# Kernel optimization log

Measured on AMD Instinct MI355X. Metric: run time of the kernel, lower is better.

## Reference

```python
import jax, jax.numpy as jnp
import numpy as np

MODEL_DIM = 1024
HIDDEN = 2048
NUM_GROUPS = 2
EXPERTS_PER_GP = 4
NUM_EXPERTS = NUM_GROUPS * EXPERTS_PER_GP
TOP_K = 2
B, T = 2, 2048


def _swiglu(x):
    a, b = jnp.split(x, 2, axis=-1)
    return jax.nn.silu(a) * b


def setup_inputs() -> dict:
    key = jax.random.key(0)
    ks = jax.random.split(key, 7)
    s = 0.02  # init scale
    return {
        "x": jax.random.normal(ks[0], (B, T, MODEL_DIM), jnp.float32),
        # torch Linear weight layout [out_features, in_features]
        "w_in": jax.random.normal(ks[1], (HIDDEN * 2, MODEL_DIM), jnp.float32) * s,   # shared_in
        "w_out": jax.random.normal(ks[2], (MODEL_DIM, HIDDEN), jnp.float32) * s,      # shared_out
        "w1": jax.random.normal(ks[3], (HIDDEN * 2, MODEL_DIM), jnp.float32) * s,     # w1_shared
        "w2": jax.random.normal(ks[4], (NUM_EXPERTS, MODEL_DIM, HIDDEN), jnp.float32) * s,  # w2_expert stack
        "wg": jax.random.normal(ks[5], (NUM_GROUPS, MODEL_DIM), jnp.float32) * s,     # group_gate
        "we": jax.random.normal(ks[6], (NUM_EXPERTS, MODEL_DIM), jnp.float32) * s,    # expert_gate
        "gb": jnp.zeros((NUM_GROUPS,), jnp.float32),   # group_bias
        "eb": jnp.zeros((NUM_EXPERTS,), jnp.float32),  # expert_bias
    }


def reference(x, w_in, w_out, w1, w2, wg, we, gb, eb):
    Bs, Ts, C = x.shape
    S = Bs * Ts
    flat = x.reshape(S, C)

    # shared expert path
    shared = _swiglu(flat @ w_in.T) @ w_out.T                    # [S, C]

    # level-1: group gate (top-1)
    g_probs = jax.nn.softmax(flat @ wg.T + gb, axis=-1)          # [S, G]
    g_idx = jnp.argmax(g_probs, axis=-1)                         # [S]

    # level-2: expert gate masked to the chosen group
    e_logits = flat @ we.T + eb                                  # [S, E]
    egid = jnp.arange(NUM_EXPERTS) // EXPERTS_PER_GP             # expert -> group id
    masked = jnp.where(g_idx[:, None] == egid[None, :], e_logits, -jnp.inf)
    e_probs = jax.nn.softmax(masked, axis=-1)                    # zero outside group

    g_prob = jnp.take_along_axis(g_probs, g_idx[:, None], axis=1)  # [S, 1]
    p_expert = e_probs * g_prob                                  # [S, E]

    topv, topi = jax.lax.top_k(p_expert, TOP_K)                  # [S, k]

    # per-token per-expert combine weight (dense [S, E], rows k-sparse)
    w_se = jnp.zeros((S, NUM_EXPERTS), x.dtype).at[
        jnp.arange(S)[:, None], topi].add(topv)

    # w1 is shared across experts -> compute hidden once for all tokens
    h = _swiglu(flat @ w1.T)                                     # [S, H]

    # routed = sum_e w_se[:, e] * (h @ w2[e].T); scale commutes through linear
    routed = jnp.zeros_like(shared)
    for e in range(NUM_EXPERTS):  # small fixed expert count
        routed = routed + (h * w_se[:, e:e + 1]) @ w2[e].T

    return (shared + routed).reshape(Bs, Ts, C)
```

## Files before the change

### kernel.cpp

```cpp
#include <hip/hip_runtime.h>
#include <math.h>


#define C_DIM 1024
#define H_DIM 2048
#define S_TOK 4096

typedef _Float16 f16x8 __attribute__((ext_vector_type(8)));
typedef float f32x4 __attribute__((ext_vector_type(4)));

#define AS3(p) ((__attribute__((address_space(3))) void*)(p))
#define AS1c(p) ((const __attribute__((address_space(1))) void*)(p))

__global__ __launch_bounds__(256) void cvt_all(
    const float* __restrict__ x, const float* __restrict__ w_in,
    const float* __restrict__ w1, const float* __restrict__ w_out,
    const float* __restrict__ w2, _Float16* __restrict__ xh,
    _Float16* __restrict__ winh, _Float16* __restrict__ w1h,
    _Float16* __restrict__ wouth, _Float16* __restrict__ w2h) {
  int i = blockIdx.x * 256 + threadIdx.x;
  const float* s; _Float16* d; int off;
  if (i < 524288)        { s = x;     d = xh;    off = i; }
  else if (i < 1048576)  { s = w_in;  d = winh;  off = i - 524288; }
  else if (i < 1572864)  { s = w1;    d = w1h;   off = i - 1048576; }
  else if (i < 1835008)  { s = w_out; d = wouth; off = i - 1572864; }
  else                   { s = w2;    d = w2h;   off = i - 1835008; }
  const float4* sp = reinterpret_cast<const float4*>(s) + (size_t)off * 2;
  float4 a = sp[0], b = sp[1];
  f16x8 h;
  h[0] = (_Float16)a.x; h[1] = (_Float16)a.y; h[2] = (_Float16)a.z; h[3] = (_Float16)a.w;
  h[4] = (_Float16)b.x; h[5] = (_Float16)b.y; h[6] = (_Float16)b.z; h[7] = (_Float16)b.w;
  reinterpret_cast<f16x8*>(d)[off] = h;
}

__global__ __launch_bounds__(256) void gate_kernel(const float* __restrict__ x,
    const float* __restrict__ wg, const float* __restrict__ we,
    const float* __restrict__ gb, const float* __restrict__ eb,
    int* __restrict__ top2_e, float* __restrict__ top2_w) {
  const int lane = threadIdx.x & 63;
  const int token = blockIdx.x * 4 + (threadIdx.x >> 6);
  const float* xr = x + (size_t)token * C_DIM + lane * 16;
  float xv[16];
#pragma unroll
  for (int i = 0; i < 16; i += 4) {
    float4 t = *reinterpret_cast<const float4*>(xr + i);
    xv[i] = t.x; xv[i + 1] = t.y; xv[i + 2] = t.z; xv[i + 3] = t.w;
  }
  float dots[10];
#pragma unroll
  for (int g = 0; g < 10; ++g) {
    const float* wr = (g < 2 ? wg + (size_t)g * C_DIM : we + (size_t)(g - 2) * C_DIM) + lane * 16;
    float d = 0.f;
#pragma unroll
    for (int i = 0; i < 16; i += 4) {
      float4 t = *reinterpret_cast<const float4*>(wr + i);
      d += xv[i] * t.x + xv[i + 1] * t.y + xv[i + 2] * t.z + xv[i + 3] * t.w;
    }
#pragma unroll
    for (int off = 32; off > 0; off >>= 1) d += __shfl_xor(d, off);
    dots[g] = d;
  }
  if (lane != 0) return;
  float g0 = dots[0] + gb[0], g1 = dots[1] + gb[1];
  int gidx = (g0 >= g1) ? 0 : 1;
  float gm = fmaxf(g0, g1);
  float ex0 = expf(g0 - gm), ex1 = expf(g1 - gm);
  float gprob = (gidx == 0 ? ex0 : ex1) / (ex0 + ex1);
  const int base = gidx * 4;
  float el[4];
  float m = -1e30f;
#pragma unroll
  for (int j = 0; j < 4; ++j) { el[j] = dots[2 + base + j] + eb[base + j]; m = fmaxf(m, el[j]); }
  float s = 0.f;
#pragma unroll
  for (int j = 0; j < 4; ++j) { el[j] = expf(el[j] - m); s += el[j]; }
  float p[8];
#pragma unroll
  for (int e = 0; e < 8; ++e) p[e] = 0.f;
#pragma unroll
  for (int j = 0; j < 4; ++j) p[base + j] = el[j] / s * gprob;
  int i1 = 0; float v1 = -1.f;
#pragma unroll
  for (int e = 0; e < 8; ++e) if (p[e] > v1) { v1 = p[e]; i1 = e; }
  int i2 = -1; float v2 = -1.f;
#pragma unroll
  for (int e = 0; e < 8; ++e) if (e != i1 && p[e] > v2) { v2 = p[e]; i2 = e; }
  top2_e[token * 2] = i1;     top2_w[token * 2] = v1;
  top2_e[token * 2 + 1] = i2; top2_w[token * 2 + 1] = v2;
}

__global__ __launch_bounds__(256) void scanfill(const int* __restrict__ top2_e,
    const float* __restrict__ top2_w, int* __restrict__ offs_g,
    int* __restrict__ tok_list, float* __restrict__ scale_list,
    int* __restrict__ tok2slot) {
  __shared__ int cnt[8], offs[9], cur[8];
  const int tid = threadIdx.x;
  if (tid < 8) { cnt[tid] = 0; cur[tid] = 0; }
  __syncthreads();
  for (int i = tid; i < 2 * S_TOK; i += 256) atomicAdd(&cnt[top2_e[i]], 1);
  __syncthreads();
  if (tid == 0) {
    offs[0] = 0;
    for (int e = 0; e < 8; ++e) offs[e + 1] = offs[e] + cnt[e];
    for (int e = 0; e < 9; ++e) offs_g[e] = offs[e];
  }
  __syncthreads();
  for (int i = tid; i < 2 * S_TOK; i += 256) {
    int e = top2_e[i];
    int slot = atomicAdd(&cur[e], 1);
    int g = offs[e] + slot;
    tok_list[g] = i >> 1;
    scale_list[g] = top2_w[i];
    tok2slot[i] = g;
  }
}

__device__ __forceinline__ void stage_tile(_Float16* lds, const _Float16* src,
                                           int ld, int tid) {
#pragma unroll
  for (int i = 0; i < 2; ++i) {
    int c = tid + i * 512;
    int row = c >> 3;
    int u = c & 7;
    const _Float16* g = src + (size_t)row * ld + ((u ^ (row & 7)) << 3);
    _Float16* l = lds + ((c & ~63) << 3);
    __builtin_amdgcn_global_load_lds(AS1c(g), AS3(l), 16, 0, 0);
  }
}

__device__ __forceinline__ f16x8 frag_ld(const _Float16* t, int row, int u) {
  return *reinterpret_cast<const f16x8*>(t + row * 64 + ((u ^ (row & 7)) << 3));
}

__global__ __launch_bounds__(512) void gemm_swiglu(const _Float16* __restrict__ A,
    const _Float16* __restrict__ W, _Float16* __restrict__ H) {
  __shared__ _Float16 At[128 * 64];
  __shared__ _Float16 Ba[128 * 64];
  __shared__ _Float16 Bb[128 * 64];
  const int tid = threadIdx.x;
  const int lane = tid & 63;
  const int wid = tid >> 6;
  const int wm = wid >> 2;
  const int wn = wid & 3;
  const int row0 = blockIdx.x * 128;
  const int col0 = blockIdx.y * 128;

  f32x4 accA[4][2] = {};
  f32x4 accB[4][2] = {};

  for (int kt = 0; kt < C_DIM; kt += 64) {
    stage_tile(At, A + (size_t)row0 * C_DIM + kt, C_DIM, tid);
    stage_tile(Ba, W + (size_t)col0 * C_DIM + kt, C_DIM, tid);
    stage_tile(Bb, W + (size_t)(col0 + H_DIM) * C_DIM + kt, C_DIM, tid);
    __syncthreads();
#pragma unroll
    for (int ks = 0; ks < 2; ++ks) {
      const int u = (ks << 2) + (lane >> 4);
      f16x8 af[4], ba[2], bb[2];
#pragma unroll
      for (int m = 0; m < 4; ++m)
        af[m] = frag_ld(At, wm * 64 + m * 16 + (lane & 15), u);
#pragma unroll
      for (int n = 0; n < 2; ++n) {
        ba[n] = frag_ld(Ba, wn * 32 + n * 16 + (lane & 15), u);
        bb[n] = frag_ld(Bb, wn * 32 + n * 16 + (lane & 15), u);
      }
#pragma unroll
      for (int m = 0; m < 4; ++m)
#pragma unroll
        for (int n = 0; n < 2; ++n) {
          accA[m][n] = __builtin_amdgcn_mfma_f32_16x16x32_f16(af[m], ba[n], accA[m][n], 0, 0, 0);
          accB[m][n] = __builtin_amdgcn_mfma_f32_16x16x32_f16(af[m], bb[n], accB[m][n], 0, 0, 0);
        }
    }
    __syncthreads();
  }
#pragma unroll
  for (int m = 0; m < 4; ++m)
#pragma unroll
    for (int n = 0; n < 2; ++n)
#pragma unroll
      for (int r = 0; r < 4; ++r) {
        int row = row0 + wm * 64 + m * 16 + ((lane >> 4) << 2) + r;
        int col = col0 + wn * 32 + n * 16 + (lane & 15);
        float a = accA[m][n][r];
        float b = accB[m][n][r];
        float hval = (a / (1.0f + expf(-a))) * b;
        H[(size_t)row * H_DIM + col] = (_Float16)hval;
      }
}

__global__ __launch_bounds__(512) void gemm_out(
    const _Float16* __restrict__ H1, const _Float16* __restrict__ H2,
    const _Float16* __restrict__ Wout, const _Float16* __restrict__ W2,
    const int* __restrict__ offs_g, const int* __restrict__ tok_list,
    const float* __restrict__ scale_list,
    float* __restrict__ out, _Float16* __restrict__ routed) {
  __shared__ _Float16 At[128 * 64];
  __shared__ _Float16 Bt[128 * 64];
  __shared__ float sse[128];
  const int tid = threadIdx.x;
  const int lane = tid & 63;
  const int wid = tid >> 6;
  const int wm = wid >> 2, wn = wid & 3;

  const int b = blockIdx.x;
  const bool shared_role = (b < 256);
  int rb, cb, offs_e = 0, n_e = 0;
  const _Float16* Bp;
  if (shared_role) {
    rb = b >> 3; cb = b & 7;
    Bp = Wout;
  } else {
    int eb = b - 256;
    int e = eb >> 8; rb = (eb >> 3) & 31; cb = eb & 7;
    offs_e = offs_g[e]; n_e = offs_g[e + 1] - offs_e;
    if (rb * 128 >= n_e) return;
    Bp = W2 + (size_t)e * C_DIM * H_DIM;
    if (tid < 128) {
      int lr = rb * 128 + tid;
      sse[tid] = (lr < n_e) ? scale_list[offs_e + lr] : 0.f;
    }
  }

  const _Float16* aptr[2];
  _Float16* ldst[2];
#pragma unroll
  for (int i = 0; i < 2; ++i) {
    int c = tid + i * 512;
    int row = c >> 3, u = c & 7;
    int swz = (u ^ (row & 7)) << 3;
    const _Float16* rowbase;
    if (shared_role) {
      rowbase = H1 + (size_t)(rb * 128 + row) * H_DIM;
    } else {
      int lr = rb * 128 + row;
      int gs = offs_e + (lr < n_e ? lr : n_e - 1);
      rowbase = H2 + (size_t)tok_list[gs] * H_DIM;
    }
    aptr[i] = rowbase + swz;
    ldst[i] = At + ((c & ~63) << 3);
  }

  f32x4 acc[4][2] = {};
  for (int kt = 0; kt < H_DIM; kt += 64) {
#pragma unroll
    for (int i = 0; i < 2; ++i)
      __builtin_amdgcn_global_load_lds(AS1c(aptr[i] + kt), AS3(ldst[i]), 16, 0, 0);
    stage_tile(Bt, Bp + (size_t)cb * 128 * H_DIM + kt, H_DIM, tid);
    __syncthreads();
#pragma unroll
    for (int ks = 0; ks < 2; ++ks) {
      const int u = (ks << 2) + (lane >> 4);
      f16x8 af[4], bf[2];
#pragma unroll
      for (int m = 0; m < 4; ++m)
        af[m] = frag_ld(At, wm * 64 + m * 16 + (lane & 15), u);
#pragma unroll
      for (int n = 0; n < 2; ++n)
        bf[n] = frag_ld(Bt, wn * 32 + n * 16 + (lane & 15), u);
#pragma unroll
      for (int m = 0; m < 4; ++m)
#pragma unroll
        for (int n = 0; n < 2; ++n)
          acc[m][n] = __builtin_amdgcn_mfma_f32_16x16x32_f16(af[m], bf[n], acc[m][n], 0, 0, 0);
    }
    __syncthreads();
  }

#pragma unroll
  for (int m = 0; m < 4; ++m)
#pragma unroll
    for (int n = 0; n < 2; ++n)
#pragma unroll
      for (int r = 0; r < 4; ++r) {
        int rloc = wm * 64 + m * 16 + ((lane >> 4) << 2) + r;
        int col = cb * 128 + wn * 32 + n * 16 + (lane & 15);
        if (shared_role) {
          out[(size_t)(rb * 128 + rloc) * C_DIM + col] = acc[m][n][r];
        } else {
          int lr = rb * 128 + rloc;
          if (lr < n_e)
            routed[(size_t)(offs_e + lr) * C_DIM + col] =
                (_Float16)(sse[rloc] * acc[m][n][r]);
        }
      }
}

__global__ __launch_bounds__(256) void combine_final(float* __restrict__ out,
    const _Float16* __restrict__ routed, const int* __restrict__ tok2slot) {
  const int t = blockIdx.x * 2 + (threadIdx.x >> 7);
  const int cp = (threadIdx.x & 127) << 3;
  const int s0 = tok2slot[t * 2], s1 = tok2slot[t * 2 + 1];
  f16x8 r0 = *reinterpret_cast<const f16x8*>(routed + (size_t)s0 * C_DIM + cp);
  f16x8 r1 = *reinterpret_cast<const f16x8*>(routed + (size_t)s1 * C_DIM + cp);
  float* op = out + (size_t)t * C_DIM + cp;
  float4 o0 = *reinterpret_cast<const float4*>(op);
  float4 o1 = *reinterpret_cast<const float4*>(op + 4);
  o0.x += (float)r0[0] + (float)r1[0];
  o0.y += (float)r0[1] + (float)r1[1];
  o0.z += (float)r0[2] + (float)r1[2];
  o0.w += (float)r0[3] + (float)r1[3];
  o1.x += (float)r0[4] + (float)r1[4];
  o1.y += (float)r0[5] + (float)r1[5];
  o1.z += (float)r0[6] + (float)r1[6];
  o1.w += (float)r0[7] + (float)r1[7];
  *reinterpret_cast<float4*>(op) = o0;
  *reinterpret_cast<float4*>(op + 4) = o1;
}

extern "C" void kernel_launch(void* const* d_in, const int* in_sizes, int n_in,
                              void* d_out, int out_size, void* d_ws, size_t ws_size,
                              hipStream_t stream) {
  const float* x     = (const float*)d_in[0];
  const float* w_in  = (const float*)d_in[1];
  const float* w_out = (const float*)d_in[2];
  const float* w1    = (const float*)d_in[3];
  const float* w2    = (const float*)d_in[4];
  const float* wg    = (const float*)d_in[5];
  const float* we    = (const float*)d_in[6];
  const float* gb    = (const float*)d_in[7];
  const float* eb    = (const float*)d_in[8];
  float* out = (float*)d_out;

  char* ws = (char*)d_ws;
  const size_t MB = 1u << 20;
  _Float16* xh     = (_Float16*)(ws + 0 * MB);
  _Float16* winh   = (_Float16*)(ws + 8 * MB);
  _Float16* routed = (_Float16*)(ws + 0 * MB);
  _Float16* w1h    = (_Float16*)(ws + 16 * MB);
  _Float16* wouth  = (_Float16*)(ws + 24 * MB);
  _Float16* w2h    = (_Float16*)(ws + 28 * MB);
  _Float16* H1     = (_Float16*)(ws + 60 * MB);
  _Float16* H2     = (_Float16*)(ws + 76 * MB);
  char* sm = ws + 92 * MB;
  int*   offs_g     = (int*)(sm);
  int*   top2_e     = (int*)(sm + 64);
  float* top2_w     = (float*)(sm + 64 + 32768);
  int*   tok_list   = (int*)(sm + 64 + 65536);
  float* scale_list = (float*)(sm + 64 + 98304);
  int*   tok2slot   = (int*)(sm + 64 + 131072);

  cvt_all<<<15360, 256, 0, stream>>>(x, w_in, w1, w_out, w2,
                                     xh, winh, w1h, wouth, w2h);
  gate_kernel<<<1024, 256, 0, stream>>>(x, wg, we, gb, eb, top2_e, top2_w);
  scanfill<<<1, 256, 0, stream>>>(top2_e, top2_w, offs_g, tok_list,
                                  scale_list, tok2slot);

  gemm_swiglu<<<dim3(32, 16), 512, 0, stream>>>(xh, winh, H1);
  gemm_swiglu<<<dim3(32, 16), 512, 0, stream>>>(xh, w1h, H2);

  gemm_out<<<2304, 512, 0, stream>>>(H1, H2, wouth, w2h, offs_g, tok_list,
                                     scale_list, out, routed);
  combine_final<<<2048, 256, 0, stream>>>(out, routed, tok2slot);
}
```

Baseline: 360.6 us.

## Fuse both SwiGLU GEMMs into one 256x256-tiled pipelined kernel with interleaved weights

```diff
diff --git a/kernel.cpp b/kernel.cpp
--- a/kernel.cpp
+++ b/kernel.cpp
@@ -16,21 +16,28 @@
     const float* __restrict__ x, const float* __restrict__ w_in,
     const float* __restrict__ w1, const float* __restrict__ w_out,
     const float* __restrict__ w2, _Float16* __restrict__ xh,
-    _Float16* __restrict__ winh, _Float16* __restrict__ w1h,
-    _Float16* __restrict__ wouth, _Float16* __restrict__ w2h) {
+    _Float16* __restrict__ wprime, _Float16* __restrict__ wouth,
+    _Float16* __restrict__ w2h) {
   int i = blockIdx.x * 256 + threadIdx.x;
-  const float* s; _Float16* d; int off;
-  if (i < 524288)        { s = x;     d = xh;    off = i; }
-  else if (i < 1048576)  { s = w_in;  d = winh;  off = i - 524288; }
-  else if (i < 1572864)  { s = w1;    d = w1h;   off = i - 1048576; }
-  else if (i < 1835008)  { s = w_out; d = wouth; off = i - 1572864; }
-  else                   { s = w2;    d = w2h;   off = i - 1835008; }
-  const float4* sp = reinterpret_cast<const float4*>(s) + (size_t)off * 2;
+  const float* s; _Float16* d; size_t soff, doff;
+  if (i < 524288) { s = x; d = xh; soff = doff = (size_t)i; }
+  else if (i < 1572864) {
+    int n = i - 524288;
+    int out_row = n >> 7, kc = n & 127;
+    int wmat = out_row >> 12, r = out_row & 4095;
+    int g = r >> 5, ii = r & 31;
+    int src_row = (ii < 16) ? (g * 16 + ii) : (2048 + g * 16 + (ii - 16));
+    s = wmat ? w1 : w_in; d = wprime;
+    soff = (size_t)src_row * 128 + kc;
+    doff = (size_t)n;
+  } else if (i < 1835008) { int n = i - 1572864; s = w_out; d = wouth; soff = doff = (size_t)n; }
+  else { int n = i - 1835008; s = w2; d = w2h; soff = doff = (size_t)n; }
+  const float4* sp = reinterpret_cast<const float4*>(s) + soff * 2;
   float4 a = sp[0], b = sp[1];
   f16x8 h;
   h[0] = (_Float16)a.x; h[1] = (_Float16)a.y; h[2] = (_Float16)a.z; h[3] = (_Float16)a.w;
   h[4] = (_Float16)b.x; h[5] = (_Float16)b.y; h[6] = (_Float16)b.z; h[7] = (_Float16)b.w;
-  reinterpret_cast<f16x8*>(d)[off] = h;
+  reinterpret_cast<f16x8*>(d)[doff] = h;
 }
 
 __global__ __launch_bounds__(256) void gate_kernel(const float* __restrict__ x,
@@ -70,15 +77,15 @@
   float el[4];
   float m = -1e30f;
 #pragma unroll
-  for (int j = 0; j < 4; ++j) { el[j] = dots[2 + base + j] + eb[base + j]; m = fmaxf(m, el[j]); }
+  for (int jj = 0; jj < 4; ++jj) { el[jj] = dots[2 + base + jj] + eb[base + jj]; m = fmaxf(m, el[jj]); }
   float s = 0.f;
 #pragma unroll
-  for (int j = 0; j < 4; ++j) { el[j] = expf(el[j] - m); s += el[j]; }
+  for (int jj = 0; jj < 4; ++jj) { el[jj] = expf(el[jj] - m); s += el[jj]; }
   float p[8];
 #pragma unroll
   for (int e = 0; e < 8; ++e) p[e] = 0.f;
 #pragma unroll
-  for (int j = 0; j < 4; ++j) p[base + j] = el[j] / s * gprob;
+  for (int jj = 0; jj < 4; ++jj) p[base + jj] = el[jj] / s * gprob;
   int i1 = 0; float v1 = -1.f;
 #pragma unroll
   for (int e = 0; e < 8; ++e) if (p[e] > v1) { v1 = p[e]; i1 = e; }
@@ -115,7 +122,7 @@
   }
 }
 
-__device__ __forceinline__ void stage_tile(_Float16* lds, const _Float16* src,
+__device__ __forceinline__ void stage_tile(_Float16* lds_, const _Float16* src,
                                            int ld, int tid) {
 #pragma unroll
   for (int i = 0; i < 2; ++i) {
@@ -123,7 +130,7 @@
     int row = c >> 3;
     int u = c & 7;
     const _Float16* g = src + (size_t)row * ld + ((u ^ (row & 7)) << 3);
-    _Float16* l = lds + ((c & ~63) << 3);
+    _Float16* l = lds_ + ((c & ~63) << 3);
     __builtin_amdgcn_global_load_lds(AS1c(g), AS3(l), 16, 0, 0);
   }
 }
@@ -132,61 +139,106 @@
   return *reinterpret_cast<const f16x8*>(t + row * 64 + ((u ^ (row & 7)) << 3));
 }
 
-__global__ __launch_bounds__(512) void gemm_swiglu(const _Float16* __restrict__ A,
-    const _Float16* __restrict__ W, _Float16* __restrict__ H) {
-  __shared__ _Float16 At[128 * 64];
-  __shared__ _Float16 Ba[128 * 64];
-  __shared__ _Float16 Bb[128 * 64];
+#define BAR __builtin_amdgcn_s_barrier()
+#define LGKM0 do { asm volatile("s_waitcnt lgkmcnt(0)" ::: "memory"); \
+                   __builtin_amdgcn_sched_barrier(0); } while (0)
+#define PRI1 __builtin_amdgcn_s_setprio(1)
+#define PRI0 __builtin_amdgcn_s_setprio(0)
+
+#define STAGEA(h_, t_) do { \
+  const _Float16* s_ = aS[h_] + (size_t)(t_) * 64; \
+  _Float16* d_ = lds + ((t_) & 1) * 32768 + (h_) * 8192 + grp0; \
+  __builtin_amdgcn_global_load_lds(AS1c(s_), AS3(d_), 16, 0, 0); \
+  __builtin_amdgcn_global_load_lds(AS1c(s_ + 65536), AS3(d_ + 4096), 16, 0, 0); \
+} while (0)
+#define STAGEB(h_, t_) do { \
+  const _Float16* s_ = bS[h_] + (size_t)(t_) * 64; \
+  _Float16* d_ = lds + ((t_) & 1) * 32768 + 16384 + (h_) * 8192 + grp0; \
+  __builtin_amdgcn_global_load_lds(AS1c(s_), AS3(d_), 16, 0, 0); \
+  __builtin_amdgcn_global_load_lds(AS1c(s_ + 65536), AS3(d_ + 4096), 16, 0, 0); \
+} while (0)
+
+#define LDA(MB_) do { _Pragma("unroll") for (int mm = 0; mm < 4; ++mm) \
+  { _Pragma("unroll") for (int ks = 0; ks < 2; ++ks) \
+    af[mm][ks] = frag_ld(At, wm * 128 + (MB_) + mm * 16 + lr, ks * 4 + lq); } } while (0)
+#define LDB(DST_, CB_) do { _Pragma("unroll") for (int nn = 0; nn < 2; ++nn) \
+  { _Pragma("unroll") for (int ks = 0; ks < 2; ++ks) \
+    DST_[nn][ks] = frag_ld(Bt, wn * 64 + (CB_) + nn * 16 + lr, ks * 4 + lq); } } while (0)
+#define QUAD(MB_, BF_, NB_) do { \
+  _Pragma("unroll") for (int ks = 0; ks < 2; ++ks) \
+  _Pragma("unroll") for (int mm = 0; mm < 4; ++mm) \
+  _Pragma("unroll") for (int nn = 0; nn < 2; ++nn) \
+    acc[(MB_) + mm][(NB_) + nn] = __builtin_amdgcn_mfma_f32_16x16x32_f16( \
+        af[mm][ks], BF_[nn][ks], acc[(MB_) + mm][(NB_) + nn], 0, 0, 0); \
+} while (0)
+
+__global__ __launch_bounds__(512, 2) void gemm_fused_swiglu(
+    const _Float16* __restrict__ A, const _Float16* __restrict__ Wp,
+    _Float16* __restrict__ H1, _Float16* __restrict__ H2) {
+  __shared__ _Float16 lds[65536];
   const int tid = threadIdx.x;
   const int lane = tid & 63;
   const int wid = tid >> 6;
-  const int wm = wid >> 2;
-  const int wn = wid & 3;
-  const int row0 = blockIdx.x * 128;
-  const int col0 = blockIdx.y * 128;
-
-  f32x4 accA[4][2] = {};
-  f32x4 accB[4][2] = {};
-
-  for (int kt = 0; kt < C_DIM; kt += 64) {
-    stage_tile(At, A + (size_t)row0 * C_DIM + kt, C_DIM, tid);
-    stage_tile(Ba, W + (size_t)col0 * C_DIM + kt, C_DIM, tid);
-    stage_tile(Bb, W + (size_t)(col0 + H_DIM) * C_DIM + kt, C_DIM, tid);
-    __syncthreads();
-#pragma unroll
-    for (int ks = 0; ks < 2; ++ks) {
-      const int u = (ks << 2) + (lane >> 4);
-      f16x8 af[4], ba[2], bb[2];
-#pragma unroll
-      for (int m = 0; m < 4; ++m)
-        af[m] = frag_ld(At, wm * 64 + m * 16 + (lane & 15), u);
-#pragma unroll
-      for (int n = 0; n < 2; ++n) {
-        ba[n] = frag_ld(Ba, wn * 32 + n * 16 + (lane & 15), u);
-        bb[n] = frag_ld(Bb, wn * 32 + n * 16 + (lane & 15), u);
-      }
-#pragma unroll
-      for (int m = 0; m < 4; ++m)
-#pragma unroll
-        for (int n = 0; n < 2; ++n) {
-          accA[m][n] = __builtin_amdgcn_mfma_f32_16x16x32_f16(af[m], ba[n], accA[m][n], 0, 0, 0);
-          accB[m][n] = __builtin_amdgcn_mfma_f32_16x16x32_f16(af[m], bb[n], accB[m][n], 0, 0, 0);
-        }
-    }
-    __syncthreads();
-  }
-#pragma unroll
-  for (int m = 0; m < 4; ++m)
-#pragma unroll
-    for (int n = 0; n < 2; ++n)
+  const int wm = wid >> 2, wn = wid & 3;
+  const int lr = lane & 15, lq = lane >> 4;
+
+  const int bid = blockIdx.x;
+  const int xcd = bid & 7, j = bid >> 3;
+  const int nb = xcd * 4 + (j & 3);
+  const int mb = j >> 2;
+  const int row0 = mb * 256;
+  const int colg0 = nb * 256;
+
+  const int rA = tid >> 3, uA = tid & 7;
+  const int grp0 = (tid & ~63) << 3;
+  const int swz = (uA ^ (rA & 7)) << 3;
+  const _Float16* aS[2];
+  const _Float16* bS[2];
+#pragma unroll
+  for (int h = 0; h < 2; ++h) {
+    aS[h] = A  + (size_t)(row0  + h * 128 + rA) * 1024 + swz;
+    bS[h] = Wp + (size_t)(colg0 + h * 128 + rA) * 1024 + swz;
+  }
+
+  STAGEB(0, 0); STAGEB(1, 0); STAGEA(0, 0); STAGEA(1, 0);
+  STAGEB(0, 1); STAGEB(1, 1); STAGEA(0, 1); STAGEA(1, 1);
+  asm volatile("s_waitcnt vmcnt(8)" ::: "memory");
+  BAR;
+
+  f32x4 acc[8][4] = {};
+  f16x8 af[4][2], bf[2][2], bf2[2][2];
+
+  for (int t = 0; t < 16; ++t) {
+    const _Float16* At = lds + (t & 1) * 32768;
+    const _Float16* Bt = At + 16384;
+    LDA(0); LDB(bf, 0);
+    BAR; LGKM0; PRI1; QUAD(0, bf, 0); PRI0; BAR;
+    LDB(bf2, 32);
+    BAR; LGKM0; PRI1; QUAD(0, bf2, 2); PRI0; BAR;
+    LDA(64);
+    if (t < 14) { STAGEB(0, t + 2); STAGEB(1, t + 2); }
+    BAR; LGKM0; PRI1; QUAD(4, bf, 0); PRI0; BAR;
+    if (t < 14) { STAGEA(0, t + 2); STAGEA(1, t + 2); }
+    BAR; PRI1; QUAD(4, bf2, 2); PRI0;
+    if (t <= 13) { asm volatile("s_waitcnt vmcnt(8)" ::: "memory"); }
+    else if (t == 14) { asm volatile("s_waitcnt vmcnt(0)" ::: "memory"); }
+    BAR;
+  }
+
+  _Float16* Hd = (colg0 >= 4096) ? H2 : H1;
+  const int col0 = colg0 & 4095;
+  const int hbase = (col0 >> 1) + wn * 32 + lr;
+#pragma unroll
+  for (int mm = 0; mm < 8; ++mm)
+#pragma unroll
+    for (int np = 0; np < 2; ++np)
 #pragma unroll
       for (int r = 0; r < 4; ++r) {
-        int row = row0 + wm * 64 + m * 16 + ((lane >> 4) << 2) + r;
-        int col = col0 + wn * 32 + n * 16 + (lane & 15);
-        float a = accA[m][n][r];
-        float b = accB[m][n][r];
-        float hval = (a / (1.0f + expf(-a))) * b;
-        H[(size_t)row * H_DIM + col] = (_Float16)hval;
+        float a = acc[mm][np * 2][r];
+        float b = acc[mm][np * 2 + 1][r];
+        float h = (a / (1.0f + expf(-a))) * b;
+        int row = row0 + wm * 128 + mm * 16 + lq * 4 + r;
+        Hd[(size_t)row * H_DIM + hbase + np * 16] = (_Float16)h;
       }
 }
 
@@ -209,17 +261,19 @@
   int rb, cb, offs_e = 0, n_e = 0;
   const _Float16* Bp;
   if (shared_role) {
-    rb = b >> 3; cb = b & 7;
+    int x = b & 7, k = b >> 3;
+    rb = x + (k >> 3) * 8; cb = k & 7;
     Bp = Wout;
   } else {
-    int eb = b - 256;
-    int e = eb >> 8; rb = (eb >> 3) & 31; cb = eb & 7;
+    int bp = b - 256;
+    int e = bp & 7, k = bp >> 3;
+    rb = k >> 3; cb = k & 7;
     offs_e = offs_g[e]; n_e = offs_g[e + 1] - offs_e;
     if (rb * 128 >= n_e) return;
     Bp = W2 + (size_t)e * C_DIM * H_DIM;
     if (tid < 128) {
-      int lr = rb * 128 + tid;
-      sse[tid] = (lr < n_e) ? scale_list[offs_e + lr] : 0.f;
+      int lrr = rb * 128 + tid;
+      sse[tid] = (lrr < n_e) ? scale_list[offs_e + lrr] : 0.f;
     }
   }
 
@@ -234,8 +288,8 @@
     if (shared_role) {
       rowbase = H1 + (size_t)(rb * 128 + row) * H_DIM;
     } else {
-      int lr = rb * 128 + row;
-      int gs = offs_e + (lr < n_e ? lr : n_e - 1);
+      int lrr = rb * 128 + row;
+      int gs = offs_e + (lrr < n_e ? lrr : n_e - 1);
       rowbase = H2 + (size_t)tok_list[gs] * H_DIM;
     }
     aptr[i] = rowbase + swz;
@@ -252,18 +306,18 @@
 #pragma unroll
     for (int ks = 0; ks < 2; ++ks) {
       const int u = (ks << 2) + (lane >> 4);
-      f16x8 af[4], bf[2];
+      f16x8 af[4], bfr[2];
 #pragma unroll
       for (int m = 0; m < 4; ++m)
         af[m] = frag_ld(At, wm * 64 + m * 16 + (lane & 15), u);
 #pragma unroll
       for (int n = 0; n < 2; ++n)
-        bf[n] = frag_ld(Bt, wn * 32 + n * 16 + (lane & 15), u);
+        bfr[n] = frag_ld(Bt, wn * 32 + n * 16 + (lane & 15), u);
 #pragma unroll
       for (int m = 0; m < 4; ++m)
 #pragma unroll
         for (int n = 0; n < 2; ++n)
-          acc[m][n] = __builtin_amdgcn_mfma_f32_16x16x32_f16(af[m], bf[n], acc[m][n], 0, 0, 0);
+          acc[m][n] = __builtin_amdgcn_mfma_f32_16x16x32_f16(af[m], bfr[n], acc[m][n], 0, 0, 0);
     }
     __syncthreads();
   }
@@ -279,9 +333,9 @@
         if (shared_role) {
           out[(size_t)(rb * 128 + rloc) * C_DIM + col] = acc[m][n][r];
         } else {
-          int lr = rb * 128 + rloc;
-          if (lr < n_e)
-            routed[(size_t)(offs_e + lr) * C_DIM + col] =
+          int lrr = rb * 128 + rloc;
+          if (lrr < n_e)
+            routed[(size_t)(offs_e + lrr) * C_DIM + col] =
                 (_Float16)(sse[rloc] * acc[m][n][r]);
         }
       }
@@ -326,9 +380,8 @@
   char* ws = (char*)d_ws;
   const size_t MB = 1u << 20;
   _Float16* xh     = (_Float16*)(ws + 0 * MB);
-  _Float16* winh   = (_Float16*)(ws + 8 * MB);
+  _Float16* wprime = (_Float16*)(ws + 8 * MB);
   _Float16* routed = (_Float16*)(ws + 0 * MB);
-  _Float16* w1h    = (_Float16*)(ws + 16 * MB);
   _Float16* wouth  = (_Float16*)(ws + 24 * MB);
   _Float16* w2h    = (_Float16*)(ws + 28 * MB);
   _Float16* H1     = (_Float16*)(ws + 60 * MB);
@@ -342,13 +395,12 @@
   int*   tok2slot   = (int*)(sm + 64 + 131072);
 
   cvt_all<<<15360, 256, 0, stream>>>(x, w_in, w1, w_out, w2,
-                                     xh, winh, w1h, wouth, w2h);
+                                     xh, wprime, wouth, w2h);
   gate_kernel<<<1024, 256, 0, stream>>>(x, wg, we, gb, eb, top2_e, top2_w);
   scanfill<<<1, 256, 0, stream>>>(top2_e, top2_w, offs_g, tok_list,
                                   scale_list, tok2slot);
 
-  gemm_swiglu<<<dim3(32, 16), 512, 0, stream>>>(xh, winh, H1);
-  gemm_swiglu<<<dim3(32, 16), 512, 0, stream>>>(xh, w1h, H2);
+  gemm_fused_swiglu<<<512, 512, 0, stream>>>(xh, wprime, H1, H2);
 
   gemm_out<<<2304, 512, 0, stream>>>(H1, H2, wouth, w2h, offs_g, tok_list,
                                      scale_list, out, routed);
```

Result: faster. 345.2 us (-4.3%).
